# Performance work log

Measured on AMD Instinct MI355X. Metric: run time of the kernel, lower is better.

Reference implementation:

```python
import jax, jax.numpy as jnp
import numpy as np

N_CAMS = 2000
N_PTS = 500000
N_OBS = 5000000


def quat_rotate(q, v):
    """Rotate vectors v [..., 3] by quaternions q [..., 4] in (x, y, z, w) order (pypose convention)."""
    qv, qw = q[..., :3], q[..., 3:4]
    uv = jnp.cross(qv, v)
    uuv = jnp.cross(qv, uv)
    return v + 2.0 * (qw * uv + uuv)


def setup_inputs() -> dict:
    key = jax.random.key(0)
    k0, k1, k2, k3, k4, k5, k6 = jax.random.split(key, 7)
    observe = jax.random.normal(k0, (N_OBS, 2), dtype=jnp.float32)
    cidx = jax.random.randint(k1, (N_OBS,), 0, N_CAMS)
    pidx = jax.random.randint(k2, (N_OBS,), 0, N_PTS)
    # Camera intrinsics: (focal, k1, k2)
    K = jnp.concatenate([
        500.0 + 10.0 * jax.random.normal(k3, (N_CAMS, 1), dtype=jnp.float32),
        0.01 * jax.random.normal(k3, (N_CAMS, 2), dtype=jnp.float32),
    ], axis=-1)
    # SE3 poses (tx,ty,tz,qx,qy,qz,qw): near-identity rotation, z-offset translation
    t = 0.1 * jax.random.normal(k4, (N_CAMS, 3), dtype=jnp.float32)
    t = t.at[:, 2].add(10.0)  # keep points in front of cameras (cp_z ~ 10)
    qv = 0.05 * jax.random.normal(k5, (N_CAMS, 3), dtype=jnp.float32)
    q = jnp.concatenate([qv, jnp.ones((N_CAMS, 1), dtype=jnp.float32)], axis=-1)
    q = q / jnp.linalg.norm(q, axis=-1, keepdims=True)
    C = jnp.concatenate([t, q], axis=-1)
    P = jax.random.normal(k6, (N_PTS, 3), dtype=jnp.float32)
    return {"observe": observe, "cidx": cidx, "pidx": pidx, "K": K, "C": C, "P": P}


def reference(observe, cidx, pidx, K, C, P):
    Kc = K[cidx]          # [N_OBS, 3]
    Cc = C[cidx]          # [N_OBS, 7]
    Pp = P[pidx]          # [N_OBS, 3]
    t, q = Cc[:, :3], Cc[:, 3:7]
    cp = quat_rotate(q, Pp) + t                    # SE3 action
    n = -cp[:, :2] / cp[:, 2:3]                    # perspective divide
    radius = jnp.sum(n * n, axis=-1, keepdims=True)
    focal, k1, k2 = Kc[:, :1], Kc[:, 1:2], Kc[:, 2:3]
    distortion = 1.0 + k1 * radius + k2 * radius * radius
    return focal * distortion * n - observe
```

## Files before the change

### kernel.cpp

```cpp
#include <hip/hip_runtime.h>


typedef int   vi4 __attribute__((ext_vector_type(4)));
typedef float vf4 __attribute__((ext_vector_type(4)));

__device__ __forceinline__ void reproj_one(
    float vx, float vy, float vz,
    vf4 r0, vf4 r1, vf4 r2,
    float obx, float oby, float* ox, float* oy)
{
    float f  = r0.x, k1 = r0.y, k2 = r0.z;
    float tx = r0.w, ty = r1.x, tz = r1.y;
    float qx = r1.z, qy = r1.w, qz = r2.x, qw = r2.y;

    float uvx = qy * vz - qz * vy;
    float uvy = qz * vx - qx * vz;
    float uvz = qx * vy - qy * vx;
    float uuvx = qy * uvz - qz * uvy;
    float uuvy = qz * uvx - qx * uvz;
    float uuvz = qx * uvy - qy * uvx;

    float cpx = vx + 2.0f * (qw * uvx + uuvx) + tx;
    float cpy = vy + 2.0f * (qw * uvy + uuvy) + ty;
    float cpz = vz + 2.0f * (qw * uvz + uuvz) + tz;

    float nx = -cpx / cpz;
    float ny = -cpy / cpz;
    float r  = nx * nx + ny * ny;

    float dist = 1.0f + k1 * r + k2 * r * r;
    float fd   = f * dist;

    *ox = fd * nx - obx;
    *oy = fd * ny - oby;
}

__global__ __launch_bounds__(1024) void reproj_kernel(
    const float*  __restrict__ observe,
    const int*    __restrict__ cidx,
    const int*    __restrict__ pidx,
    const float*  __restrict__ K,
    const float*  __restrict__ C,
    const float*  __restrict__ P,
    float*        __restrict__ out,
    int n, int ncams)
{
    extern __shared__ float cam_lds[];

    for (int c = threadIdx.x; c < ncams; c += 1024) {
        const float* Kc = K + 3 * c;
        const float* Cc = C + 7 * c;
        float* r = cam_lds + 12 * c;
        r[0] = Kc[0]; r[1] = Kc[1]; r[2] = Kc[2];
        r[3] = Cc[0]; r[4] = Cc[1]; r[5] = Cc[2];
        r[6] = Cc[3]; r[7] = Cc[4]; r[8] = Cc[5]; r[9] = Cc[6];
    }
    __syncthreads();

    int base = (blockIdx.x * 1024 + threadIdx.x) * 4;
    if (base >= n) return;

    if (base + 4 <= n) {
        vi4 c4 = __builtin_nontemporal_load((const vi4*)(cidx + base));
        vi4 p4 = __builtin_nontemporal_load((const vi4*)(pidx + base));
        vf4 ob01 = __builtin_nontemporal_load((const vf4*)(observe + 2 * base));
        vf4 ob23 = __builtin_nontemporal_load((const vf4*)(observe + 2 * base + 4));

        int ci[4] = { c4.x, c4.y, c4.z, c4.w };
        int pi[4] = { p4.x, p4.y, p4.z, p4.w };

        float v[4][3];
        #pragma unroll
        for (int k = 0; k < 4; ++k) {
            const float* Pp = P + 3 * pi[k];
            v[k][0] = Pp[0]; v[k][1] = Pp[1]; v[k][2] = Pp[2];
        }

        float res[8];
        #pragma unroll
        for (int k = 0; k < 4; ++k) {
            const vf4* camv = (const vf4*)(cam_lds + 12 * ci[k]);
            vf4 r0 = camv[0], r1 = camv[1], r2 = camv[2];
            float obx = (k == 0) ? ob01.x : (k == 1) ? ob01.z : (k == 2) ? ob23.x : ob23.z;
            float oby = (k == 0) ? ob01.y : (k == 1) ? ob01.w : (k == 2) ? ob23.y : ob23.w;
            reproj_one(v[k][0], v[k][1], v[k][2], r0, r1, r2,
                       obx, oby, &res[2 * k], &res[2 * k + 1]);
        }

        vf4 o0 = { res[0], res[1], res[2], res[3] };
        vf4 o1 = { res[4], res[5], res[6], res[7] };
        __builtin_nontemporal_store(o0, (vf4*)(out + 2 * base));
        __builtin_nontemporal_store(o1, (vf4*)(out + 2 * base + 4));
    } else {
        for (int i = base; i < n; ++i) {
            int c = cidx[i];
            int p = pidx[i];
            const vf4* camv = (const vf4*)(cam_lds + 12 * c);
            vf4 r0 = camv[0], r1 = camv[1], r2 = camv[2];
            const float* Pp = P + 3 * p;
            float ox, oy;
            reproj_one(Pp[0], Pp[1], Pp[2], r0, r1, r2,
                       observe[2 * i], observe[2 * i + 1], &ox, &oy);
            out[2 * i]     = ox;
            out[2 * i + 1] = oy;
        }
    }
}

extern "C" void kernel_launch(void* const* d_in, const int* in_sizes, int n_in,
                              void* d_out, int out_size, void* d_ws, size_t ws_size,
                              hipStream_t stream)
{
    const float* observe = (const float*)d_in[0];
    const int*   cidx    = (const int*)d_in[1];
    const int*   pidx    = (const int*)d_in[2];
    const float* K       = (const float*)d_in[3];
    const float* C       = (const float*)d_in[4];
    const float* P       = (const float*)d_in[5];
    float*       out     = (float*)d_out;

    int n     = in_sizes[1];
    int ncams = in_sizes[3] / 3;

    int block = 1024;
    int obs_per_block = block * 4;
    int grid = (n + obs_per_block - 1) / obs_per_block;
    size_t lds_bytes = (size_t)ncams * 12 * sizeof(float);

    reproj_kernel<<<grid, block, lds_bytes, stream>>>(
        observe, cidx, pidx, K, C, P, out, n, ncams);
}
```

Before: 70.01 us.

## Use grid-stride persistent blocks, split camera LDS into SoA, vectorize point loads

The launch now uses at most 512 blocks in a grid-stride loop, so each block loads the camera table into LDS once and reuses it over many observations instead of about 1221 blocks each reloading it. Camera data is stored in LDS as separate quaternion, translation+focal and distortion arrays, which cuts per-camera LDS from 12 to 10 floats. Point coordinates are read with a 3-float vector load, and launch bounds ask the compiler for higher occupancy. The cost is fewer blocks, which could reduce latency hiding for the random gathers, plus possible register pressure from the occupancy hint.

```diff
diff --git a/kernel.cpp b/kernel.cpp
--- a/kernel.cpp
+++ b/kernel.cpp
@@ -3,15 +3,17 @@
 
 typedef int   vi4 __attribute__((ext_vector_type(4)));
 typedef float vf4 __attribute__((ext_vector_type(4)));
+typedef float vf2 __attribute__((ext_vector_type(2)));
+typedef float vf3 __attribute__((ext_vector_type(3), aligned(4)));
 
 __device__ __forceinline__ void reproj_one(
     float vx, float vy, float vz,
-    vf4 r0, vf4 r1, vf4 r2,
+    vf4 q, vf4 tf, vf2 d,
     float obx, float oby, float* ox, float* oy)
 {
-    float f  = r0.x, k1 = r0.y, k2 = r0.z;
-    float tx = r0.w, ty = r1.x, tz = r1.y;
-    float qx = r1.z, qy = r1.w, qz = r2.x, qw = r2.y;
+    float qx = q.x, qy = q.y, qz = q.z, qw = q.w;
+    float tx = tf.x, ty = tf.y, tz = tf.z, f = tf.w;
+    float k1 = d.x, k2 = d.y;
 
     float uvx = qy * vz - qz * vy;
     float uvy = qz * vx - qx * vz;
@@ -35,7 +37,7 @@
     *oy = fd * ny - oby;
 }
 
-__global__ __launch_bounds__(1024) void reproj_kernel(
+__global__ __launch_bounds__(1024, 8) void reproj_kernel(
     const float*  __restrict__ observe,
     const int*    __restrict__ cidx,
     const int*    __restrict__ pidx,
@@ -45,64 +47,64 @@
     float*        __restrict__ out,
     int n, int ncams)
 {
-    extern __shared__ float cam_lds[];
+    extern __shared__ float lds[];
+    vf4* Qs = (vf4*)lds;
+    vf4* Ts = (vf4*)(lds + 4 * ncams);
+    vf2* Ds = (vf2*)(lds + 8 * ncams);
 
     for (int c = threadIdx.x; c < ncams; c += 1024) {
+        const float* Cc = C + 7 * c;
         const float* Kc = K + 3 * c;
-        const float* Cc = C + 7 * c;
-        float* r = cam_lds + 12 * c;
-        r[0] = Kc[0]; r[1] = Kc[1]; r[2] = Kc[2];
-        r[3] = Cc[0]; r[4] = Cc[1]; r[5] = Cc[2];
-        r[6] = Cc[3]; r[7] = Cc[4]; r[8] = Cc[5]; r[9] = Cc[6];
+        vf4 q  = { Cc[3], Cc[4], Cc[5], Cc[6] };
+        vf4 tf = { Cc[0], Cc[1], Cc[2], Kc[0] };
+        vf2 d  = { Kc[1], Kc[2] };
+        Qs[c] = q; Ts[c] = tf; Ds[c] = d;
     }
     __syncthreads();
 
-    int base = (blockIdx.x * 1024 + threadIdx.x) * 4;
-    if (base >= n) return;
+    int tid    = blockIdx.x * 1024 + threadIdx.x;
+    int stride = gridDim.x * 1024 * 4;
 
-    if (base + 4 <= n) {
-        vi4 c4 = __builtin_nontemporal_load((const vi4*)(cidx + base));
-        vi4 p4 = __builtin_nontemporal_load((const vi4*)(pidx + base));
-        vf4 ob01 = __builtin_nontemporal_load((const vf4*)(observe + 2 * base));
-        vf4 ob23 = __builtin_nontemporal_load((const vf4*)(observe + 2 * base + 4));
+    for (int base = tid * 4; base < n; base += stride) {
+        if (base + 4 <= n) {
+            vi4 c4 = __builtin_nontemporal_load((const vi4*)(cidx + base));
+            vi4 p4 = __builtin_nontemporal_load((const vi4*)(pidx + base));
+            vf4 ob01 = __builtin_nontemporal_load((const vf4*)(observe + 2 * base));
+            vf4 ob23 = __builtin_nontemporal_load((const vf4*)(observe + 2 * base + 4));
 
-        int ci[4] = { c4.x, c4.y, c4.z, c4.w };
-        int pi[4] = { p4.x, p4.y, p4.z, p4.w };
+            int ci[4] = { c4.x, c4.y, c4.z, c4.w };
+            int pi[4] = { p4.x, p4.y, p4.z, p4.w };
 
-        float v[4][3];
-        #pragma unroll
-        for (int k = 0; k < 4; ++k) {
-            const float* Pp = P + 3 * pi[k];
-            v[k][0] = Pp[0]; v[k][1] = Pp[1]; v[k][2] = Pp[2];
-        }
+            vf3 v0 = *(const vf3*)(P + 3 * pi[0]);
+            vf3 v1 = *(const vf3*)(P + 3 * pi[1]);
+            vf3 v2 = *(const vf3*)(P + 3 * pi[2]);
+            vf3 v3 = *(const vf3*)(P + 3 * pi[3]);
 
-        float res[8];
-        #pragma unroll
-        for (int k = 0; k < 4; ++k) {
-            const vf4* camv = (const vf4*)(cam_lds + 12 * ci[k]);
-            vf4 r0 = camv[0], r1 = camv[1], r2 = camv[2];
-            float obx = (k == 0) ? ob01.x : (k == 1) ? ob01.z : (k == 2) ? ob23.x : ob23.z;
-            float oby = (k == 0) ? ob01.y : (k == 1) ? ob01.w : (k == 2) ? ob23.y : ob23.w;
-            reproj_one(v[k][0], v[k][1], v[k][2], r0, r1, r2,
-                       obx, oby, &res[2 * k], &res[2 * k + 1]);
-        }
+            float res[8];
+            reproj_one(v0.x, v0.y, v0.z, Qs[ci[0]], Ts[ci[0]], Ds[ci[0]],
+                       ob01.x, ob01.y, &res[0], &res[1]);
+            reproj_one(v1.x, v1.y, v1.z, Qs[ci[1]], Ts[ci[1]], Ds[ci[1]],
+                       ob01.z, ob01.w, &res[2], &res[3]);
+            reproj_one(v2.x, v2.y, v2.z, Qs[ci[2]], Ts[ci[2]], Ds[ci[2]],
+                       ob23.x, ob23.y, &res[4], &res[5]);
+            reproj_one(v3.x, v3.y, v3.z, Qs[ci[3]], Ts[ci[3]], Ds[ci[3]],
+                       ob23.z, ob23.w, &res[6], &res[7]);
 
-        vf4 o0 = { res[0], res[1], res[2], res[3] };
-        vf4 o1 = { res[4], res[5], res[6], res[7] };
-        __builtin_nontemporal_store(o0, (vf4*)(out + 2 * base));
-        __builtin_nontemporal_store(o1, (vf4*)(out + 2 * base + 4));
-    } else {
-        for (int i = base; i < n; ++i) {
-            int c = cidx[i];
-            int p = pidx[i];
-            const vf4* camv = (const vf4*)(cam_lds + 12 * c);
-            vf4 r0 = camv[0], r1 = camv[1], r2 = camv[2];
-            const float* Pp = P + 3 * p;
-            float ox, oy;
-            reproj_one(Pp[0], Pp[1], Pp[2], r0, r1, r2,
-                       observe[2 * i], observe[2 * i + 1], &ox, &oy);
-            out[2 * i]     = ox;
-            out[2 * i + 1] = oy;
+            vf4 o0 = { res[0], res[1], res[2], res[3] };
+            vf4 o1 = { res[4], res[5], res[6], res[7] };
+            __builtin_nontemporal_store(o0, (vf4*)(out + 2 * base));
+            __builtin_nontemporal_store(o1, (vf4*)(out + 2 * base + 4));
+        } else {
+            for (int i = base; i < n; ++i) {
+                int c = cidx[i];
+                int p = pidx[i];
+                vf3 pv = *(const vf3*)(P + 3 * p);
+                float ox, oy;
+                reproj_one(pv.x, pv.y, pv.z, Qs[c], Ts[c], Ds[c],
+                           observe[2 * i], observe[2 * i + 1], &ox, &oy);
+                out[2 * i]     = ox;
+                out[2 * i + 1] = oy;
+            }
         }
     }
 }
@@ -123,9 +125,10 @@
     int ncams = in_sizes[3] / 3;
 
     int block = 1024;
-    int obs_per_block = block * 4;
-    int grid = (n + obs_per_block - 1) / obs_per_block;
-    size_t lds_bytes = (size_t)ncams * 12 * sizeof(float);
+    int grid = 512;
+    int need = (n + block * 4 - 1) / (block * 4);
+    if (grid > need) grid = need;
+    size_t lds_bytes = (size_t)ncams * 10 * sizeof(float);
 
     reproj_kernel<<<grid, block, lds_bytes, stream>>>(
         observe, cidx, pidx, K, C, P, out, n, ncams);
```

Result: no change. 71.08 us (+1.5%).
